# Performance work log

Hardware: AMD Instinct MI355X
Metric: run time of the kernel (lower is better)

The kernel has to match this reference:

```python
import jax, jax.numpy as jnp
import numpy as np


def setup_inputs() -> dict:
    key = jax.random.key(0)
    kx, kw = jax.random.split(key)
    B, IN, OUT = 8192, 1024, 4096
    x = jax.random.normal(kx, (B, IN), dtype=jnp.float32)
    # torch.rand -> uniform [0,1)
    weight = jax.random.uniform(kw, (IN, OUT), dtype=jnp.float32)
    return {"x": x, "weight": weight}


def reference(x, weight):
    # Faithful to: (x.unsqueeze(-1) - weight).pow(2).sum(-2)
    # i.e. out[b, o] = sum_i (x[b, i] - weight[i, o])**2
    # Computed via the squared-distance expansion to avoid the
    # (B, in, out) broadcast intermediate:
    x_sq = jnp.sum(x * x, axis=-1, keepdims=True)          # (B, 1)
    w_sq = jnp.sum(weight * weight, axis=0)                # (OUT,)
    cross = jnp.matmul(x, weight)                          # (B, OUT)
    return x_sq - 2.0 * cross + w_sq
```

## Files before the change

kernel.cpp:

```cpp
#include <hip/hip_runtime.h>
#include <cstdint>
#include <cstddef>

#define B_DIM   8192
#define IN_DIM  1024
#define OUT_DIM 4096
#define KT2     (IN_DIM / 64)

typedef __attribute__((ext_vector_type(8)))  int   i32x8;
typedef __attribute__((ext_vector_type(4)))  int   i32x4;
typedef __attribute__((ext_vector_type(16))) float f32x16;

__device__ __forceinline__ void async_copy16(const void* gptr, void* ldsptr) {
    __builtin_amdgcn_global_load_lds(
        (__attribute__((address_space(1))) void*)gptr,
        (__attribute__((address_space(3))) void*)ldsptr,
        16, 0, 0);
}

__device__ __forceinline__ int pack4_fp8(float a, float b, float c, float d) {
    int pk = __builtin_amdgcn_cvt_pk_fp8_f32(a, b, 0, false);
    pk = __builtin_amdgcn_cvt_pk_fp8_f32(c, d, pk, true);
    return pk;
}


__global__ __launch_bounds__(512) void tile_x_kernel(
    const float* __restrict__ x, unsigned char* __restrict__ At,
    float* __restrict__ xsq, float* __restrict__ wsq)
{
    const int t = threadIdx.x;
    const int w = t >> 6;
    const int l = t & 63;
    const int mt = blockIdx.x;
    const int m  = mt * 32 + (l & 31);

    float s = 0.0f;
    #pragma unroll
    for (int c = 0; c < 2; ++c) {
        const int kt2 = c * 8 + w;
        const float* src = x + (size_t)m * IN_DIM + kt2 * 64 + (l >> 5) * 32;
        i32x4 lo, hi;
        #pragma unroll
        for (int j = 0; j < 4; ++j) {
            float4 v = ((const float4*)src)[j];
            s += v.x*v.x + v.y*v.y + v.z*v.z + v.w*v.w;
            lo[j] = pack4_fp8(v.x, v.y, v.z, v.w);
        }
        #pragma unroll
        for (int j = 0; j < 4; ++j) {
            float4 v = ((const float4*)src)[4 + j];
            s += v.x*v.x + v.y*v.y + v.z*v.z + v.w*v.w;
            hi[j] = pack4_fp8(v.x, v.y, v.z, v.w);
        }
        unsigned char* pan = At + ((size_t)mt * KT2 + kt2) * 2048;
        *(i32x4*)(pan + l * 16)        = lo;
        *(i32x4*)(pan + 1024 + l * 16) = hi;
    }
    s += __shfl_down(s, 32, 64);
    __shared__ float red[8][32];
    if (l < 32) red[w][l] = s;
    __syncthreads();
    if (t < 32) {
        float r = 0.0f;
        #pragma unroll
        for (int j = 0; j < 8; ++j) r += red[j][t];
        xsq[mt * 32 + t] = r;
    }

    if (blockIdx.x < 8) wsq[blockIdx.x * 512 + t] = 0.0f;
}

__global__ __launch_bounds__(256) void tile_w_kernel(
    const float* __restrict__ wgt, unsigned char* __restrict__ Bt,
    float* __restrict__ wsq)
{
    __shared__ float tile[256 * 33];
    const int t  = threadIdx.x;
    const int w  = t >> 6;
    const int l  = t & 63;
    const int nt = blockIdx.x;
    const int q  = blockIdx.y;
    const int n0 = nt * 32;

    {
        const int rbase = t >> 2, cg = (t & 3) * 8;
        #pragma unroll
        for (int rep = 0; rep < 4; ++rep) {
            const int r = rbase + rep * 64;
            const float* src = wgt + (size_t)(q * 256 + r) * OUT_DIM + n0 + cg;
            float4 v0 = ((const float4*)src)[0];
            float4 v1 = ((const float4*)src)[1];
            float* d = &tile[r * 33 + cg];
            d[0] = v0.x; d[1] = v0.y; d[2] = v0.z; d[3] = v0.w;
            d[4] = v1.x; d[5] = v1.y; d[6] = v1.z; d[7] = v1.w;
        }
    }
    __syncthreads();

    const int kt2 = q * 4 + w;
    const int n   = l & 31;
    const int kb  = w * 64 + (l >> 5) * 32;
    float s = 0.0f;
    i32x4 lo, hi;
    #pragma unroll
    for (int j4 = 0; j4 < 4; ++j4) {
        float f0 = tile[(kb + j4 * 4 + 0) * 33 + n];
        float f1 = tile[(kb + j4 * 4 + 1) * 33 + n];
        float f2 = tile[(kb + j4 * 4 + 2) * 33 + n];
        float f3 = tile[(kb + j4 * 4 + 3) * 33 + n];
        s += f0*f0 + f1*f1 + f2*f2 + f3*f3;
        lo[j4] = pack4_fp8(f0, f1, f2, f3);
    }
    #pragma unroll
    for (int j4 = 0; j4 < 4; ++j4) {
        float f0 = tile[(kb + 16 + j4 * 4 + 0) * 33 + n];
        float f1 = tile[(kb + 16 + j4 * 4 + 1) * 33 + n];
        float f2 = tile[(kb + 16 + j4 * 4 + 2) * 33 + n];
        float f3 = tile[(kb + 16 + j4 * 4 + 3) * 33 + n];
        s += f0*f0 + f1*f1 + f2*f2 + f3*f3;
        hi[j4] = pack4_fp8(f0, f1, f2, f3);
    }
    unsigned char* pan = Bt + ((size_t)nt * KT2 + kt2) * 2048;
    *(i32x4*)(pan + l * 16)        = lo;
    *(i32x4*)(pan + 1024 + l * 16) = hi;

    s += __shfl_down(s, 32, 64);
    __shared__ float red[4][32];
    if (l < 32) red[w][l] = s;
    __syncthreads();
    if (t < 32) atomicAdd(&wsq[n0 + t], red[0][t] + red[1][t] + red[2][t] + red[3][t]);
}

__global__ __launch_bounds__(512, 2) void rbf_gemm_kernel(
    const unsigned char* __restrict__ At,
    const unsigned char* __restrict__ Bt,
    const float* __restrict__ xsq,
    const float* __restrict__ wsq,
    float* __restrict__ out)
{
    __shared__ __align__(16) unsigned char sm[3][32768];

    const int t    = threadIdx.x;
    const int w    = t >> 6;
    const int l    = t & 63;
    const int l32  = l & 31;
    const int half = l >> 5;
    const int waveRow = w >> 2;
    const int waveCol = w & 3;

    const int wg  = blockIdx.y * 32 + blockIdx.x;
    const int swz = (wg & 7) * 64 + (wg >> 3);
    const int bm  = swz >> 4;
    const int bn  = swz & 15;

    f32x16 acc[4][2];
    #pragma unroll
    for (int mi = 0; mi < 4; ++mi)
        #pragma unroll
        for (int ni = 0; ni < 2; ++ni)
            #pragma unroll
            for (int r = 0; r < 16; ++r)
                acc[mi][ni][r] = 0.0f;

    const unsigned char* gaBase = At + (size_t)(bm * 8 + w) * (KT2 * 2048);
    const unsigned char* gbBase = Bt + (size_t)(bn * 8 + w) * (KT2 * 2048);

    auto stage = [&](unsigned char* base, int k) {
        const unsigned char* ga = gaBase + k * 2048;
        const unsigned char* gb = gbBase + k * 2048;
        unsigned char* As = base + w * 2048;
        unsigned char* Bs = base + 16384 + w * 2048;
        #pragma unroll
        for (int h = 0; h < 2; ++h) {
            async_copy16(ga + h * 1024 + l * 16, As + h * 1024);
            async_copy16(gb + h * 1024 + l * 16, Bs + h * 1024);
        }
    };

    auto ldfrag = [&](const unsigned char* base, int p) -> i32x8 {
        i32x4 lo = *(const i32x4*)(base + p * 2048 + l * 16);
        i32x4 hi = *(const i32x4*)(base + p * 2048 + 1024 + l * 16);
        i32x8 r;
        r[0] = lo[0]; r[1] = lo[1]; r[2] = lo[2]; r[3] = lo[3];
        r[4] = hi[0]; r[5] = hi[1]; r[6] = hi[2]; r[7] = hi[3];
        return r;
    };

    stage(sm[0], 0);
    stage(sm[1], 1);

    int cb = 0, sb = 2;
    for (int k = 0; k < 16; ++k) {
        if (k < 15) asm volatile("s_waitcnt vmcnt(4)" ::: "memory");
        else        asm volatile("s_waitcnt vmcnt(0)" ::: "memory");
        __builtin_amdgcn_s_barrier();
        __builtin_amdgcn_sched_barrier(0);

        if (k <= 13) stage(sm[sb], k + 2);

        const unsigned char* As = sm[cb];
        const unsigned char* Bs = sm[cb] + 16384;
        i32x8 bf0 = ldfrag(Bs, waveCol * 2 + 0);
        i32x8 bf1 = ldfrag(Bs, waveCol * 2 + 1);
        i32x8 af[4];
        #pragma unroll
        for (int mi = 0; mi < 4; ++mi)
            af[mi] = ldfrag(As, waveRow * 4 + mi);

        __builtin_amdgcn_s_setprio(1);
        #pragma unroll
        for (int mi = 0; mi < 4; ++mi) {
            acc[mi][0] = __builtin_amdgcn_mfma_scale_f32_32x32x64_f8f6f4(
                af[mi], bf0, acc[mi][0],
                0, 0,
                0, 0x7F7F7F7F,
                0, 0x7F7F7F7F);
            acc[mi][1] = __builtin_amdgcn_mfma_scale_f32_32x32x64_f8f6f4(
                af[mi], bf1, acc[mi][1],
                0, 0, 0, 0x7F7F7F7F, 0, 0x7F7F7F7F);
        }
        __builtin_amdgcn_s_setprio(0);

        cb = (cb == 2) ? 0 : cb + 1;
        sb = (sb == 2) ? 0 : sb + 1;
    }

    const int ncol = bn * 256 + waveCol * 64 + l32;
    const float wsn0 = wsq[ncol];
    const float wsn1 = wsq[ncol + 32];
    #pragma unroll
    for (int mi = 0; mi < 4; ++mi) {
        const int mbase = bm * 256 + waveRow * 128 + mi * 32 + 4 * half;
        #pragma unroll
        for (int r2 = 0; r2 < 4; ++r2) {
            #pragma unroll
            for (int r1 = 0; r1 < 4; ++r1) {
                const int m  = mbase + r1 + 8 * r2;
                const float xs = xsq[m];
                float* orow = out + (size_t)m * OUT_DIM + ncol;
                orow[0]  = xs + wsn0 - 2.0f * acc[mi][0][r2 * 4 + r1];
                orow[32] = xs + wsn1 - 2.0f * acc[mi][1][r2 * 4 + r1];
            }
        }
    }
}

extern "C" void kernel_launch(void* const* d_in, const int* in_sizes, int n_in,
                              void* d_out, int out_size, void* d_ws, size_t ws_size,
                              hipStream_t stream)
{
    const float* x   = (const float*)d_in[0];
    const float* wgt = (const float*)d_in[1];
    float* out = (float*)d_out;
    char*  ws  = (char*)d_ws;

    unsigned char* At = (unsigned char*)ws;
    unsigned char* Bt = (unsigned char*)(ws + (size_t)B_DIM * IN_DIM);
    float* xsq = (float*)(ws + (size_t)B_DIM * IN_DIM + (size_t)OUT_DIM * IN_DIM);
    float* wsq = xsq + B_DIM;

    tile_x_kernel<<<B_DIM / 32, 512, 0, stream>>>(x, At, xsq, wsq);
    tile_w_kernel<<<dim3(OUT_DIM / 32, 4), 256, 0, stream>>>(wgt, Bt, wsq);
    rbf_gemm_kernel<<<dim3(32, 16), 512, 0, stream>>>(At, Bt, xsq, wsq, out);
}
```

Before: 197.6 us.

## Fuse quantize prologues and FP8 GEMM into one cooperative persistent kernel

Merges the x-quantize, w-quantize and GEMM kernels into a single cooperative launch of 256 blocks, with a grid-wide sync between the prologue and the GEMM phase. Each block now computes two output tiles in sequence. The w-norm atomics are replaced by two partial-sum arrays that are added together in the epilogue. This removes two kernel launches and the atomic traffic, but the grid is capped at 256 blocks of 512 threads (2 per CU) and adds the cost of a grid barrier.

```diff
diff --git a/kernel.cpp b/kernel.cpp
--- a/kernel.cpp
+++ b/kernel.cpp
@@ -1,4 +1,5 @@
 #include <hip/hip_runtime.h>
+#include <hip/hip_cooperative_groups.h>
 #include <cstdint>
 #include <cstddef>
 
@@ -25,224 +26,219 @@
 }
 
 
-__global__ __launch_bounds__(512) void tile_x_kernel(
-    const float* __restrict__ x, unsigned char* __restrict__ At,
-    float* __restrict__ xsq, float* __restrict__ wsq)
+__global__ __launch_bounds__(512, 2) void rbf_fused_kernel(
+    const float* __restrict__ x,
+    const float* __restrict__ wgt,
+    unsigned char* __restrict__ At,
+    unsigned char* __restrict__ Bt,
+    float* __restrict__ xsq,
+    float* __restrict__ wsq2,
+    float* __restrict__ out)
 {
+    __shared__ __align__(16) unsigned char smem[98304];
+
     const int t = threadIdx.x;
     const int w = t >> 6;
     const int l = t & 63;
-    const int mt = blockIdx.x;
-    const int m  = mt * 32 + (l & 31);
-
-    float s = 0.0f;
-    #pragma unroll
-    for (int c = 0; c < 2; ++c) {
-        const int kt2 = c * 8 + w;
-        const float* src = x + (size_t)m * IN_DIM + kt2 * 64 + (l >> 5) * 32;
-        i32x4 lo, hi;
-        #pragma unroll
-        for (int j = 0; j < 4; ++j) {
-            float4 v = ((const float4*)src)[j];
-            s += v.x*v.x + v.y*v.y + v.z*v.z + v.w*v.w;
-            lo[j] = pack4_fp8(v.x, v.y, v.z, v.w);
-        }
-        #pragma unroll
-        for (int j = 0; j < 4; ++j) {
-            float4 v = ((const float4*)src)[4 + j];
-            s += v.x*v.x + v.y*v.y + v.z*v.z + v.w*v.w;
-            hi[j] = pack4_fp8(v.x, v.y, v.z, v.w);
-        }
-        unsigned char* pan = At + ((size_t)mt * KT2 + kt2) * 2048;
-        *(i32x4*)(pan + l * 16)        = lo;
-        *(i32x4*)(pan + 1024 + l * 16) = hi;
+    const int b = blockIdx.x;
+
+    {
+        const int m = b * 32 + (l & 31);
+        float s = 0.0f;
+        #pragma unroll
+        for (int c = 0; c < 2; ++c) {
+            const int kt2 = c * 8 + w;
+            const float* src = x + (size_t)m * IN_DIM + kt2 * 64 + (l >> 5) * 32;
+            i32x4 lo, hi;
+            #pragma unroll
+            for (int j = 0; j < 4; ++j) {
+                float4 v = ((const float4*)src)[j];
+                s += v.x*v.x + v.y*v.y + v.z*v.z + v.w*v.w;
+                lo[j] = pack4_fp8(v.x, v.y, v.z, v.w);
+            }
+            #pragma unroll
+            for (int j = 0; j < 4; ++j) {
+                float4 v = ((const float4*)src)[4 + j];
+                s += v.x*v.x + v.y*v.y + v.z*v.z + v.w*v.w;
+                hi[j] = pack4_fp8(v.x, v.y, v.z, v.w);
+            }
+            unsigned char* pan = At + ((size_t)b * KT2 + kt2) * 2048;
+            *(i32x4*)(pan + l * 16)        = lo;
+            *(i32x4*)(pan + 1024 + l * 16) = hi;
+        }
+        s += __shfl_down(s, 32, 64);
+        float* red = (float*)smem;
+        if (l < 32) red[w * 32 + l] = s;
+        __syncthreads();
+        if (t < 32) {
+            float r = 0.0f;
+            #pragma unroll
+            for (int j = 0; j < 8; ++j) r += red[j * 32 + t];
+            xsq[b * 32 + t] = r;
+        }
+        __syncthreads();
     }
-    s += __shfl_down(s, 32, 64);
-    __shared__ float red[8][32];
-    if (l < 32) red[w][l] = s;
-    __syncthreads();
-    if (t < 32) {
-        float r = 0.0f;
-        #pragma unroll
-        for (int j = 0; j < 8; ++j) r += red[j][t];
-        xsq[mt * 32 + t] = r;
-    }
-
-    if (blockIdx.x < 8) wsq[blockIdx.x * 512 + t] = 0.0f;
-}
-
-__global__ __launch_bounds__(256) void tile_w_kernel(
-    const float* __restrict__ wgt, unsigned char* __restrict__ Bt,
-    float* __restrict__ wsq)
-{
-    __shared__ float tile[256 * 33];
-    const int t  = threadIdx.x;
-    const int w  = t >> 6;
-    const int l  = t & 63;
-    const int nt = blockIdx.x;
-    const int q  = blockIdx.y;
-    const int n0 = nt * 32;
 
     {
-        const int rbase = t >> 2, cg = (t & 3) * 8;
+        const int nt = b & 127, qh = b >> 7, n0 = nt * 32;
+        float* tile = (float*)smem;
+        const int rb = t >> 2, cg = (t & 3) * 8;
         #pragma unroll
         for (int rep = 0; rep < 4; ++rep) {
-            const int r = rbase + rep * 64;
-            const float* src = wgt + (size_t)(q * 256 + r) * OUT_DIM + n0 + cg;
+            const int r = rb + rep * 128;
+            const float* src = wgt + (size_t)(qh * 512 + r) * OUT_DIM + n0 + cg;
             float4 v0 = ((const float4*)src)[0];
             float4 v1 = ((const float4*)src)[1];
             float* d = &tile[r * 33 + cg];
             d[0] = v0.x; d[1] = v0.y; d[2] = v0.z; d[3] = v0.w;
             d[4] = v1.x; d[5] = v1.y; d[6] = v1.z; d[7] = v1.w;
         }
+        __syncthreads();
+
+        const int n  = l & 31;
+        const int kb = w * 64 + (l >> 5) * 32;
+        float s = 0.0f;
+        i32x4 lo, hi;
+        #pragma unroll
+        for (int j4 = 0; j4 < 4; ++j4) {
+            float f0 = tile[(kb + j4 * 4 + 0) * 33 + n];
+            float f1 = tile[(kb + j4 * 4 + 1) * 33 + n];
+            float f2 = tile[(kb + j4 * 4 + 2) * 33 + n];
+            float f3 = tile[(kb + j4 * 4 + 3) * 33 + n];
+            s += f0*f0 + f1*f1 + f2*f2 + f3*f3;
+            lo[j4] = pack4_fp8(f0, f1, f2, f3);
+        }
+        #pragma unroll
+        for (int j4 = 0; j4 < 4; ++j4) {
+            float f0 = tile[(kb + 16 + j4 * 4 + 0) * 33 + n];
+            float f1 = tile[(kb + 16 + j4 * 4 + 1) * 33 + n];
+            float f2 = tile[(kb + 16 + j4 * 4 + 2) * 33 + n];
+            float f3 = tile[(kb + 16 + j4 * 4 + 3) * 33 + n];
+            s += f0*f0 + f1*f1 + f2*f2 + f3*f3;
+            hi[j4] = pack4_fp8(f0, f1, f2, f3);
+        }
+        unsigned char* pan = Bt + ((size_t)nt * KT2 + qh * 8 + w) * 2048;
+        *(i32x4*)(pan + l * 16)        = lo;
+        *(i32x4*)(pan + 1024 + l * 16) = hi;
+
+        s += __shfl_down(s, 32, 64);
+        float* red = (float*)(smem + 67584);
+        if (l < 32) red[w * 32 + l] = s;
+        __syncthreads();
+        if (t < 32) {
+            float r = 0.0f;
+            #pragma unroll
+            for (int j = 0; j < 8; ++j) r += red[j * 32 + t];
+            wsq2[qh * OUT_DIM + n0 + t] = r;
+        }
     }
-    __syncthreads();
-
-    const int kt2 = q * 4 + w;
-    const int n   = l & 31;
-    const int kb  = w * 64 + (l >> 5) * 32;
-    float s = 0.0f;
-    i32x4 lo, hi;
-    #pragma unroll
-    for (int j4 = 0; j4 < 4; ++j4) {
-        float f0 = tile[(kb + j4 * 4 + 0) * 33 + n];
-        float f1 = tile[(kb + j4 * 4 + 1) * 33 + n];
-        float f2 = tile[(kb + j4 * 4 + 2) * 33 + n];
-        float f3 = tile[(kb + j4 * 4 + 3) * 33 + n];
-        s += f0*f0 + f1*f1 + f2*f2 + f3*f3;
-        lo[j4] = pack4_fp8(f0, f1, f2, f3);
-    }
-    #pragma unroll
-    for (int j4 = 0; j4 < 4; ++j4) {
-        float f0 = tile[(kb + 16 + j4 * 4 + 0) * 33 + n];
-        float f1 = tile[(kb + 16 + j4 * 4 + 1) * 33 + n];
-        float f2 = tile[(kb + 16 + j4 * 4 + 2) * 33 + n];
-        float f3 = tile[(kb + 16 + j4 * 4 + 3) * 33 + n];
-        s += f0*f0 + f1*f1 + f2*f2 + f3*f3;
-        hi[j4] = pack4_fp8(f0, f1, f2, f3);
-    }
-    unsigned char* pan = Bt + ((size_t)nt * KT2 + kt2) * 2048;
-    *(i32x4*)(pan + l * 16)        = lo;
-    *(i32x4*)(pan + 1024 + l * 16) = hi;
-
-    s += __shfl_down(s, 32, 64);
-    __shared__ float red[4][32];
-    if (l < 32) red[w][l] = s;
-    __syncthreads();
-    if (t < 32) atomicAdd(&wsq[n0 + t], red[0][t] + red[1][t] + red[2][t] + red[3][t]);
-}
-
-__global__ __launch_bounds__(512, 2) void rbf_gemm_kernel(
-    const unsigned char* __restrict__ At,
-    const unsigned char* __restrict__ Bt,
-    const float* __restrict__ xsq,
-    const float* __restrict__ wsq,
-    float* __restrict__ out)
-{
-    __shared__ __align__(16) unsigned char sm[3][32768];
-
-    const int t    = threadIdx.x;
-    const int w    = t >> 6;
-    const int l    = t & 63;
+
+    __threadfence();
+    cooperative_groups::this_grid().sync();
+
     const int l32  = l & 31;
     const int half = l >> 5;
     const int waveRow = w >> 2;
     const int waveCol = w & 3;
 
-    const int wg  = blockIdx.y * 32 + blockIdx.x;
-    const int swz = (wg & 7) * 64 + (wg >> 3);
-    const int bm  = swz >> 4;
-    const int bn  = swz & 15;
-
-    f32x16 acc[4][2];
-    #pragma unroll
-    for (int mi = 0; mi < 4; ++mi)
-        #pragma unroll
-        for (int ni = 0; ni < 2; ++ni)
-            #pragma unroll
-            for (int r = 0; r < 16; ++r)
-                acc[mi][ni][r] = 0.0f;
+    const int swz = (b & 7) * 32 + (b >> 3);
+    const int bm  = swz >> 3;
+    const int bnp = swz & 7;
 
     const unsigned char* gaBase = At + (size_t)(bm * 8 + w) * (KT2 * 2048);
-    const unsigned char* gbBase = Bt + (size_t)(bn * 8 + w) * (KT2 * 2048);
-
-    auto stage = [&](unsigned char* base, int k) {
-        const unsigned char* ga = gaBase + k * 2048;
-        const unsigned char* gb = gbBase + k * 2048;
-        unsigned char* As = base + w * 2048;
-        unsigned char* Bs = base + 16384 + w * 2048;
-        #pragma unroll
-        for (int h = 0; h < 2; ++h) {
-            async_copy16(ga + h * 1024 + l * 16, As + h * 1024);
-            async_copy16(gb + h * 1024 + l * 16, Bs + h * 1024);
-        }
-    };
-
-    auto ldfrag = [&](const unsigned char* base, int p) -> i32x8 {
-        i32x4 lo = *(const i32x4*)(base + p * 2048 + l * 16);
-        i32x4 hi = *(const i32x4*)(base + p * 2048 + 1024 + l * 16);
-        i32x8 r;
-        r[0] = lo[0]; r[1] = lo[1]; r[2] = lo[2]; r[3] = lo[3];
-        r[4] = hi[0]; r[5] = hi[1]; r[6] = hi[2]; r[7] = hi[3];
-        return r;
-    };
-
-    stage(sm[0], 0);
-    stage(sm[1], 1);
-
-    int cb = 0, sb = 2;
-    for (int k = 0; k < 16; ++k) {
-        if (k < 15) asm volatile("s_waitcnt vmcnt(4)" ::: "memory");
-        else        asm volatile("s_waitcnt vmcnt(0)" ::: "memory");
-        __builtin_amdgcn_s_barrier();
-        __builtin_amdgcn_sched_barrier(0);
-
-        if (k <= 13) stage(sm[sb], k + 2);
-
-        const unsigned char* As = sm[cb];
-        const unsigned char* Bs = sm[cb] + 16384;
-        i32x8 bf0 = ldfrag(Bs, waveCol * 2 + 0);
-        i32x8 bf1 = ldfrag(Bs, waveCol * 2 + 1);
-        i32x8 af[4];
+
+    for (int tt = 0; tt < 2; ++tt) {
+        const int bn = bnp * 2 + tt;
+        const unsigned char* gbBase = Bt + (size_t)(bn * 8 + w) * (KT2 * 2048);
+
+        f32x16 acc[4][2];
         #pragma unroll
         for (int mi = 0; mi < 4; ++mi)
-            af[mi] = ldfrag(As, waveRow * 4 + mi);
-
-        __builtin_amdgcn_s_setprio(1);
+            #pragma unroll
+            for (int ni = 0; ni < 2; ++ni)
+                #pragma unroll
+                for (int r = 0; r < 16; ++r)
+                    acc[mi][ni][r] = 0.0f;
+
+        auto stage = [&](unsigned char* base, int k) {
+            const unsigned char* ga = gaBase + k * 2048;
+            const unsigned char* gb = gbBase + k * 2048;
+            unsigned char* As = base + w * 2048;
+            unsigned char* Bs = base + 16384 + w * 2048;
+            #pragma unroll
+            for (int h = 0; h < 2; ++h) {
+                async_copy16(ga + h * 1024 + l * 16, As + h * 1024);
+                async_copy16(gb + h * 1024 + l * 16, Bs + h * 1024);
+            }
+        };
+
+        auto ldfrag = [&](const unsigned char* base, int p) -> i32x8 {
+            i32x4 lo = *(const i32x4*)(base + p * 2048 + l * 16);
+            i32x4 hi = *(const i32x4*)(base + p * 2048 + 1024 + l * 16);
+            i32x8 r;
+            r[0] = lo[0]; r[1] = lo[1]; r[2] = lo[2]; r[3] = lo[3];
+            r[4] = hi[0]; r[5] = hi[1]; r[6] = hi[2]; r[7] = hi[3];
+            return r;
+        };
+
+        stage(smem, 0);
+        stage(smem + 32768, 1);
+
+        int cb = 0, sb = 2;
+        for (int k = 0; k < 16; ++k) {
+            if (k < 15) asm volatile("s_waitcnt vmcnt(4)" ::: "memory");
+            else        asm volatile("s_waitcnt vmcnt(0)" ::: "memory");
+            __builtin_amdgcn_s_barrier();
+            __builtin_amdgcn_sched_barrier(0);
+
+            if (k <= 13) stage(smem + sb * 32768, k + 2);
+
+            const unsigned char* As = smem + cb * 32768;
+            const unsigned char* Bs = As + 16384;
+            i32x8 bf0 = ldfrag(Bs, waveCol * 2 + 0);
+            i32x8 bf1 = ldfrag(Bs, waveCol * 2 + 1);
+            i32x8 af[4];
+            #pragma unroll
+            for (int mi = 0; mi < 4; ++mi)
+                af[mi] = ldfrag(As, waveRow * 4 + mi);
+
+            __builtin_amdgcn_s_setprio(1);
+            #pragma unroll
+            for (int mi = 0; mi < 4; ++mi) {
+                acc[mi][0] = __builtin_amdgcn_mfma_scale_f32_32x32x64_f8f6f4(
+                    af[mi], bf0, acc[mi][0],
+                    0, 0,
+                    0, 0x7F7F7F7F,
+                    0, 0x7F7F7F7F);
+                acc[mi][1] = __builtin_amdgcn_mfma_scale_f32_32x32x64_f8f6f4(
+                    af[mi], bf1, acc[mi][1],
+                    0, 0, 0, 0x7F7F7F7F, 0, 0x7F7F7F7F);
+            }
+            __builtin_amdgcn_s_setprio(0);
+
+            cb = (cb == 2) ? 0 : cb + 1;
+            sb = (sb == 2) ? 0 : sb + 1;
+        }
+
+        const int ncol = bn * 256 + waveCol * 64 + l32;
+        const float wsn0 = wsq2[ncol]      + wsq2[OUT_DIM + ncol];
+        const float wsn1 = wsq2[ncol + 32] + wsq2[OUT_DIM + ncol + 32];
         #pragma unroll
         for (int mi = 0; mi < 4; ++mi) {
-            acc[mi][0] = __builtin_amdgcn_mfma_scale_f32_32x32x64_f8f6f4(
-                af[mi], bf0, acc[mi][0],
-                0, 0,
-                0, 0x7F7F7F7F,
-                0, 0x7F7F7F7F);
-            acc[mi][1] = __builtin_amdgcn_mfma_scale_f32_32x32x64_f8f6f4(
-                af[mi], bf1, acc[mi][1],
-                0, 0, 0, 0x7F7F7F7F, 0, 0x7F7F7F7F);
-        }
-        __builtin_amdgcn_s_setprio(0);
-
-        cb = (cb == 2) ? 0 : cb + 1;
-        sb = (sb == 2) ? 0 : sb + 1;
-    }
-
-    const int ncol = bn * 256 + waveCol * 64 + l32;
-    const float wsn0 = wsq[ncol];
-    const float wsn1 = wsq[ncol + 32];
-    #pragma unroll
-    for (int mi = 0; mi < 4; ++mi) {
-        const int mbase = bm * 256 + waveRow * 128 + mi * 32 + 4 * half;
-        #pragma unroll
-        for (int r2 = 0; r2 < 4; ++r2) {
-            #pragma unroll
-            for (int r1 = 0; r1 < 4; ++r1) {
-                const int m  = mbase + r1 + 8 * r2;
-                const float xs = xsq[m];
-                float* orow = out + (size_t)m * OUT_DIM + ncol;
-                orow[0]  = xs + wsn0 - 2.0f * acc[mi][0][r2 * 4 + r1];
-                orow[32] = xs + wsn1 - 2.0f * acc[mi][1][r2 * 4 + r1];
-            }
-        }
+            const int mbase = bm * 256 + waveRow * 128 + mi * 32 + 4 * half;
+            #pragma unroll
+            for (int r2 = 0; r2 < 4; ++r2) {
+                #pragma unroll
+                for (int r1 = 0; r1 < 4; ++r1) {
+                    const int m  = mbase + r1 + 8 * r2;
+                    const float xs = xsq[m];
+                    float* orow = out + (size_t)m * OUT_DIM + ncol;
+                    orow[0]  = xs + wsn0 - 2.0f * acc[mi][0][r2 * 4 + r1];
+                    orow[32] = xs + wsn1 - 2.0f * acc[mi][1][r2 * 4 + r1];
+                }
+            }
+        }
+        __syncthreads();
     }
 }
 
@@ -257,10 +253,11 @@
 
     unsigned char* At = (unsigned char*)ws;
     unsigned char* Bt = (unsigned char*)(ws + (size_t)B_DIM * IN_DIM);
-    float* xsq = (float*)(ws + (size_t)B_DIM * IN_DIM + (size_t)OUT_DIM * IN_DIM);
-    float* wsq = xsq + B_DIM;
-
-    tile_x_kernel<<<B_DIM / 32, 512, 0, stream>>>(x, At, xsq, wsq);
-    tile_w_kernel<<<dim3(OUT_DIM / 32, 4), 256, 0, stream>>>(wgt, Bt, wsq);
-    rbf_gemm_kernel<<<dim3(32, 16), 512, 0, stream>>>(At, Bt, xsq, wsq, out);
-}
+    float* xsq  = (float*)(ws + (size_t)B_DIM * IN_DIM + (size_t)OUT_DIM * IN_DIM);
+    float* wsq2 = xsq + B_DIM;
+
+    void* args[] = {(void*)&x, (void*)&wgt, (void*)&At, (void*)&Bt,
+                    (void*)&xsq, (void*)&wsq2, (void*)&out};
+    hipLaunchCooperativeKernel(reinterpret_cast<void*>(rbf_fused_kernel),
+                               dim3(256), dim3(512), args, 0, stream);
+}
```

Measured after the change: 335.2 us. 1.7x slower.
